# Kernel tuning notes

Hardware: AMD Instinct MI355X
Metric: run time of the kernel (lower is better)

The kernel has to match this reference:

```python
import jax, jax.numpy as jnp
import numpy as np

B, G, P, E, H, K = 16, 512, 512, 256, 16, 16
CLIP = 10.0

def setup_inputs() -> dict:
    key = jax.random.key(0)
    ks = jax.random.split(key, 10)
    d = {
        "input1": jax.random.normal(ks[0], (B, 1, E), jnp.float32),
        "input2": jax.random.normal(ks[1], (B, G, E), jnp.float32),
        "current_time": jax.random.uniform(ks[2], (B, G, 1), jnp.float32),
        "ninf_mask": jnp.zeros((B, G, P), jnp.float32),
        "encoded_nodes": jax.random.normal(ks[3], (B, P, E), jnp.float32),
        # learned params (Linear weights stored [in, out]; y = x @ W)
        "Wq": jax.random.normal(ks[4], (2 * E + 1, H * K), jnp.float32) / np.sqrt(2 * E + 1),
        "Wk": jax.random.normal(ks[5], (E, H * K), jnp.float32) / np.sqrt(E),
        "Wv": jax.random.normal(ks[6], (E, H * K), jnp.float32) / np.sqrt(E),
        "Wc_w": jax.random.normal(ks[7], (H * K, E), jnp.float32) / np.sqrt(H * K),
        "Wc_b": jax.random.normal(ks[8], (E,), jnp.float32) * 0.01,
    }
    return d

def _heads(x):  # [B, N, H*K] -> [B, H, N, K]
    b, n, _ = x.shape
    return x.reshape(b, n, H, K).transpose(0, 2, 1, 3)

def reference(input1, input2, current_time, ninf_mask, encoded_nodes, Wq, Wk, Wv, Wc_w, Wc_b):
    # reset(): precompute k, v, single_head_key from encoded_nodes
    k = _heads(encoded_nodes @ Wk)  # [B,H,P,K]
    v = _heads(encoded_nodes @ Wv)  # [B,H,P,K]

    # forward()
    input_cat = jnp.concatenate(
        (jnp.broadcast_to(input1, (B, G, E)), input2, current_time), axis=2)  # [B,G,2E+1]
    q = _heads(input_cat @ Wq)  # [B,H,G,K]

    # MHA with additive ninf mask
    score = jnp.einsum("bhgk,bhpk->bhgp", q, k) / np.sqrt(K)
    score = score + ninf_mask[:, None, :, :]
    weights = jax.nn.softmax(score, axis=3)
    out = jnp.einsum("bhgp,bhpk->bhgk", weights, v)
    out_concat = out.transpose(0, 2, 1, 3).reshape(B, G, H * K)
    mh_atten_out = out_concat @ Wc_w + Wc_b  # [B,G,E]

    # single-head pointer score with tanh clipping
    score2 = jnp.einsum("bge,bpe->bgp", mh_atten_out, encoded_nodes) / np.sqrt(E)
    score_clipped = CLIP * jnp.tanh(score2)
    probs = jax.nn.softmax(score_clipped + ninf_mask, axis=2)
    return probs
```

## Files before the change

### kernel.cpp

```cpp
#include <hip/hip_runtime.h>
#include <math.h>

#define BB 16
#define GG 512
#define PP 512
#define EE 256
#define HH 16
#define KD 16
#define HK 256

typedef __bf16 bf16x8 __attribute__((ext_vector_type(8)));
typedef __bf16 bf16x4 __attribute__((ext_vector_type(4)));
typedef float f32x4 __attribute__((ext_vector_type(4)));
typedef float f32x16 __attribute__((ext_vector_type(16)));
typedef int i32x4 __attribute__((ext_vector_type(4)));

#define SA_STRIDE 40
#define SMEM_BYTES 30720

__device__ inline void cvt_split8(const float* __restrict__ p, bf16x8& h, bf16x8& l)
{
    float4 f0 = *(const float4*)p;
    float4 f1 = *(const float4*)(p + 4);
    float v[8] = {f0.x, f0.y, f0.z, f0.w, f1.x, f1.y, f1.z, f1.w};
#pragma unroll
    for (int j = 0; j < 8; ++j) {
        __bf16 hh = (__bf16)v[j];
        h[j] = hh;
        l[j] = (__bf16)(v[j] - (float)hh);
    }
}

__device__ inline int cvt_pk_bf16(float lo, float hi)
{
    int r;
    asm("v_cvt_pk_bf16_f32 %0, %1, %2" : "=v"(r) : "v"(lo), "v"(hi));
    return r;
}

__device__ inline void w2proj_body(int bx, int tid, unsigned char* smem,
                                   const float* __restrict__ enc,
                                   const float* __restrict__ Wc,
                                   const float* __restrict__ bias,
                                   __bf16* __restrict__ W2th,
                                   __bf16* __restrict__ W2tl,
                                   float* __restrict__ biasEnc)
{
    __bf16* sAh = (__bf16*)smem;
    __bf16* sAl = sAh + 64 * SA_STRIDE;
    __bf16* sBh = sAl + 64 * SA_STRIDE;
    __bf16* sBl = sBh + 64 * SA_STRIDE;

    const int lane = tid & 63;
    const int w = __builtin_amdgcn_readfirstlane(tid >> 6);
    const int b  = bx >> 5;
    const int t  = bx & 31;
    const int p0 = (t >> 2) * 64;
    const int n0 = (t & 3) * 64;
    const bool do_bias = (n0 == 0);
    const int wm = (w >> 1) * 32, wn = (w & 1) * 32;
    const int ln = lane & 15, kq = (lane >> 4) * 8;
    const int ar = tid >> 2, ac = (tid & 3) * 8;

    f32x4 acc[2][2];
#pragma unroll
    for (int i = 0; i < 2; ++i)
#pragma unroll
        for (int j = 0; j < 2; ++j) acc[i][j] = (f32x4){0.f, 0.f, 0.f, 0.f};
    float bacc = 0.f;

    for (int k0 = 0; k0 < EE; k0 += 32) {
        {
            const float* ap = enc + ((size_t)(b * PP + p0 + ar)) * EE + k0 + ac;
            float4 f0 = *(const float4*)ap;
            float4 f1 = *(const float4*)(ap + 4);
            float v[8] = {f0.x, f0.y, f0.z, f0.w, f1.x, f1.y, f1.z, f1.w};
            bf16x8 h8, l8;
#pragma unroll
            for (int j = 0; j < 8; ++j) {
                __bf16 hh = (__bf16)v[j];
                h8[j] = hh;
                l8[j] = (__bf16)(v[j] - (float)hh);
            }
            if (do_bias) {
#pragma unroll
                for (int j = 0; j < 8; ++j) bacc += v[j] * bias[k0 + ac + j];
            }
            *(bf16x8*)&sAh[ar * SA_STRIDE + ac] = h8;
            *(bf16x8*)&sAl[ar * SA_STRIDE + ac] = l8;
        }
        {
            bf16x8 h8, l8;
            cvt_split8(Wc + (size_t)(n0 + ar) * EE + k0 + ac, h8, l8);
            *(bf16x8*)&sBh[ar * SA_STRIDE + ac] = h8;
            *(bf16x8*)&sBl[ar * SA_STRIDE + ac] = l8;
        }
        __syncthreads();

        bf16x8 ah[2], al[2];
#pragma unroll
        for (int mt = 0; mt < 2; ++mt) {
            ah[mt] = *(const bf16x8*)&sAh[(wm + mt * 16 + ln) * SA_STRIDE + kq];
            al[mt] = *(const bf16x8*)&sAl[(wm + mt * 16 + ln) * SA_STRIDE + kq];
        }
#pragma unroll
        for (int nt = 0; nt < 2; ++nt) {
            const int rowb = wn + nt * 16 + ln;
            bf16x8 bh8 = *(const bf16x8*)&sBh[rowb * SA_STRIDE + kq];
            bf16x8 bl8 = *(const bf16x8*)&sBl[rowb * SA_STRIDE + kq];
#pragma unroll
            for (int mt = 0; mt < 2; ++mt) {
                acc[mt][nt] = __builtin_amdgcn_mfma_f32_16x16x32_bf16(ah[mt], bh8, acc[mt][nt], 0, 0, 0);
                acc[mt][nt] = __builtin_amdgcn_mfma_f32_16x16x32_bf16(al[mt], bh8, acc[mt][nt], 0, 0, 0);
                acc[mt][nt] = __builtin_amdgcn_mfma_f32_16x16x32_bf16(ah[mt], bl8, acc[mt][nt], 0, 0, 0);
            }
        }
        __syncthreads();
    }

    if (do_bias) {
        bacc += __shfl_xor(bacc, 1);
        bacc += __shfl_xor(bacc, 2);
        if ((tid & 3) == 0) biasEnc[b * PP + p0 + ar] = bacc;
    }

    const int rbase = (lane >> 4) * 4;
#pragma unroll
    for (int mt = 0; mt < 2; ++mt)
#pragma unroll
        for (int nt = 0; nt < 2; ++nt)
#pragma unroll
            for (int r = 0; r < 4; ++r) {
                const int p = p0 + wm + mt * 16 + rbase + r;
                const int n = n0 + wn + nt * 16 + ln;
                const float v = acc[mt][nt][r];
                const __bf16 h = (__bf16)v;
                const size_t o = ((size_t)(b * PP + p)) * HK + n;
                W2th[o] = h;
                W2tl[o] = (__bf16)(v - (float)h);
            }
}

__global__ __launch_bounds__(256) void weight_prep(const float* __restrict__ Wk,
                                                   const float* __restrict__ Wv,
                                                   const float* __restrict__ Wq,
                                                   const float* __restrict__ Wc,
                                                   const float* __restrict__ in1,
                                                   const float* __restrict__ enc,
                                                   const float* __restrict__ Wcb,
                                                   __bf16* __restrict__ wkt_h, __bf16* __restrict__ wkt_l,
                                                   __bf16* __restrict__ wvt_h, __bf16* __restrict__ wvt_l,
                                                   __bf16* __restrict__ wqt_h, __bf16* __restrict__ wqt_l,
                                                   float* __restrict__ q1p,
                                                   __bf16* __restrict__ W2th, __bf16* __restrict__ W2tl,
                                                   float* __restrict__ biasEnc)
{
    __shared__ __align__(16) unsigned char smem[4 * 64 * SA_STRIDE * 2];
    if (blockIdx.x < 512) {
        w2proj_body(blockIdx.x, threadIdx.x, smem, enc, Wc, Wcb, W2th, W2tl, biasEnc);
        return;
    }
    int gid = (blockIdx.x - 512) * 256 + threadIdx.x;
    if (gid < 16384) {
        const int b = gid >> 10, q = (gid >> 8) & 3, n = gid & 255;
        const float* ip = in1 + (size_t)b * EE + q * 64;
        const float* wp = Wq + (size_t)(q * 64) * HK + n;
        float acc = 0.f;
#pragma unroll 8
        for (int k = 0; k < 64; ++k) acc += ip[k] * wp[(size_t)k * HK];
        q1p[gid] = acc;
        return;
    }
    int id = gid - 16384;
    if (id >= 196608) return;
    const float* W;
    __bf16 *th, *tl;
    int krow = 0;
    if (id < 65536)       { W = Wk; th = wkt_h; tl = wkt_l; }
    else if (id < 131072) { id -= 65536;  W = Wv; th = wvt_h; tl = wvt_l; }
    else                  { id -= 131072; W = Wq; th = wqt_h; tl = wqt_l; krow = 256; }
    const int k = id & 255;
    const int n = id >> 8;
    const float v = W[(size_t)(k + krow) * HK + n];
    const __bf16 h = (__bf16)v;
    th[(n << 8) + k] = h;
    tl[(n << 8) + k] = (__bf16)(v - (float)h);
}

__device__ inline void kvproj_body(int bx, int tid, unsigned char* smem,
                                   const float* __restrict__ A,
                                   const __bf16* __restrict__ Bkh,
                                   const __bf16* __restrict__ Bkl,
                                   const __bf16* __restrict__ Bvh,
                                   const __bf16* __restrict__ Bvl,
                                   __bf16* __restrict__ Khi,
                                   __bf16* __restrict__ Klo,
                                   __bf16* __restrict__ Vt)
{
    __bf16* sAh = (__bf16*)smem;
    __bf16* sAl = sAh + 64 * SA_STRIDE;
    __bf16* sB  = sAl + 64 * SA_STRIDE;

    const int lane = tid & 63;
    const int w = __builtin_amdgcn_readfirstlane(tid >> 6);
    const int m0 = (bx >> 2) * 64;
    const int n0 = (bx & 3) * 64;
    const int wm = (w >> 1) * 32, wn = (w & 1) * 32;
    const int ln = lane & 15, kq = (lane >> 4) * 8;
    const int ar = tid >> 2, ac = (tid & 3) * 8;

    const __bf16* bsel = (w == 0) ? Bkh : (w == 1) ? Bkl : (w == 2) ? Bvh : Bvl;

    f32x4 ak[2][2], av[2][2];
#pragma unroll
    for (int i = 0; i < 2; ++i)
#pragma unroll
        for (int j = 0; j < 2; ++j) {
            ak[i][j] = (f32x4){0.f, 0.f, 0.f, 0.f};
            av[i][j] = (f32x4){0.f, 0.f, 0.f, 0.f};
        }

    for (int k0 = 0; k0 < EE; k0 += 32) {
        {
            bf16x8 h8, l8;
            cvt_split8(A + (size_t)(m0 + ar) * EE + k0 + ac, h8, l8);
            *(bf16x8*)&sAh[ar * SA_STRIDE + ac] = h8;
            *(bf16x8*)&sAl[ar * SA_STRIDE + ac] = l8;
        }
        {
            const __bf16* src = bsel + (size_t)(n0 + lane) * EE + k0;
            __bf16* dst = sB + (w * 64 + lane) * SA_STRIDE;
            *(bf16x8*)&dst[0]  = *(const bf16x8*)&src[0];
            *(bf16x8*)&dst[8]  = *(const bf16x8*)&src[8];
            *(bf16x8*)&dst[16] = *(const bf16x8*)&src[16];
            *(bf16x8*)&dst[24] = *(const bf16x8*)&src[24];
        }
        __syncthreads();

        bf16x8 ah[2], al[2];
#pragma unroll
        for (int mt = 0; mt < 2; ++mt) {
            ah[mt] = *(const bf16x8*)&sAh[(wm + mt * 16 + ln) * SA_STRIDE + kq];
            al[mt] = *(const bf16x8*)&sAl[(wm + mt * 16 + ln) * SA_STRIDE + kq];
        }
#pragma unroll
        for (int nt = 0; nt < 2; ++nt) {
            const int rowb = wn + nt * 16 + ln;
            bf16x8 bkh8 = *(const bf16x8*)&sB[(0 * 64 + rowb) * SA_STRIDE + kq];
            bf16x8 bkl8 = *(const bf16x8*)&sB[(1 * 64 + rowb) * SA_STRIDE + kq];
            bf16x8 bvh8 = *(const bf16x8*)&sB[(2 * 64 + rowb) * SA_STRIDE + kq];
            bf16x8 bvl8 = *(const bf16x8*)&sB[(3 * 64 + rowb) * SA_STRIDE + kq];
#pragma unroll
            for (int mt = 0; mt < 2; ++mt) {
                ak[mt][nt] = __builtin_amdgcn_mfma_f32_16x16x32_bf16(ah[mt], bkh8, ak[mt][nt], 0, 0, 0);
                ak[mt][nt] = __builtin_amdgcn_mfma_f32_16x16x32_bf16(al[mt], bkh8, ak[mt][nt], 0, 0, 0);
                ak[mt][nt] = __builtin_amdgcn_mfma_f32_16x16x32_bf16(ah[mt], bkl8, ak[mt][nt], 0, 0, 0);
                av[mt][nt] = __builtin_amdgcn_mfma_f32_16x16x32_bf16(ah[mt], bvh8, av[mt][nt], 0, 0, 0);
                av[mt][nt] = __builtin_amdgcn_mfma_f32_16x16x32_bf16(al[mt], bvh8, av[mt][nt], 0, 0, 0);
                av[mt][nt] = __builtin_amdgcn_mfma_f32_16x16x32_bf16(ah[mt], bvl8, av[mt][nt], 0, 0, 0);
            }
        }
        __syncthreads();
    }

    __bf16* eKh = (__bf16*)smem;
    __bf16* eKl = eKh + 5120;
    __bf16* eV  = eKl + 5120;

    const int rbase = (lane >> 4) * 4;
#pragma unroll
    for (int mt = 0; mt < 2; ++mt)
#pragma unroll
        for (int nt = 0; nt < 2; ++nt) {
            const int hloc = (w & 1) * 2 + nt;
            const int nl = wn + nt * 16 + ln;
#pragma unroll
            for (int r = 0; r < 4; ++r) {
                const int m = wm + mt * 16 + rbase + r;
                const float vk = ak[mt][nt][r];
                const __bf16 hk = (__bf16)vk;
                eKh[(hloc * 64 + m) * 20 + ln] = hk;
                eKl[(hloc * 64 + m) * 20 + ln] = (__bf16)(vk - (float)hk);
                eV[nl * 68 + m] = (__bf16)av[mt][nt][r];
            }
        }
    __syncthreads();

    const int b = m0 >> 9;
    const int pbase = m0 & (PP - 1);
    {
        const int hl = tid >> 6, p = tid & 63;
        const int hg = (n0 >> 4) + hl;
        const size_t dst = (((size_t)b * HH + hg) * PP + pbase + p) * KD;
        const int base = (hl * 64 + p) * 20;
        uint2 a0 = *(const uint2*)&eKh[base + 0];
        uint2 a1 = *(const uint2*)&eKh[base + 4];
        uint2 a2 = *(const uint2*)&eKh[base + 8];
        uint2 a3 = *(const uint2*)&eKh[base + 12];
        *(uint4*)(Khi + dst)     = make_uint4(a0.x, a0.y, a1.x, a1.y);
        *(uint4*)(Khi + dst + 8) = make_uint4(a2.x, a2.y, a3.x, a3.y);
        uint2 c0 = *(const uint2*)&eKl[base + 0];
        uint2 c1 = *(const uint2*)&eKl[base + 4];
        uint2 c2 = *(const uint2*)&eKl[base + 8];
        uint2 c3 = *(const uint2*)&eKl[base + 12];
        *(uint4*)(Klo + dst)     = make_uint4(c0.x, c0.y, c1.x, c1.y);
        *(uint4*)(Klo + dst + 8) = make_uint4(c2.x, c2.y, c3.x, c3.y);
    }
    {
        const int n = tid >> 2, qq = tid & 3;
        const int ng = n0 + n, hg = ng >> 4, kk = ng & 15;
        const int base = n * 68 + qq * 16;
        uint2 v0 = *(const uint2*)&eV[base + 0];
        uint2 v1 = *(const uint2*)&eV[base + 4];
        uint2 v2 = *(const uint2*)&eV[base + 8];
        uint2 v3 = *(const uint2*)&eV[base + 12];
        const size_t dst = ((((size_t)b * HH + hg) * KD + kk) * PP) + pbase + qq * 16;
        *(uint4*)(Vt + dst)     = make_uint4(v0.x, v0.y, v1.x, v1.y);
        *(uint4*)(Vt + dst + 8) = make_uint4(v2.x, v2.y, v3.x, v3.y);
    }
}

__device__ inline void qproj_body(int bx, int tid, unsigned char* smem,
                                  const float* __restrict__ in2,
                                  const float* __restrict__ ct,
                                  const __bf16* __restrict__ Bh,
                                  const __bf16* __restrict__ Bl,
                                  const float* __restrict__ WqFull,
                                  const float* __restrict__ q1p,
                                  __bf16* __restrict__ Qhi,
                                  __bf16* __restrict__ Qlo)
{
    __bf16* sAh = (__bf16*)smem;
    __bf16* sAl = sAh + 64 * SA_STRIDE;
    __bf16* sB  = sAl + 64 * SA_STRIDE;

    const int lane = tid & 63;
    const int w = __builtin_amdgcn_readfirstlane(tid >> 6);
    const int m0 = (bx >> 2) * 64;
    const int n0 = (bx & 3) * 64;
    const int wm = (w >> 1) * 32, wn = (w & 1) * 32;
    const int ln = lane & 15, kq = (lane >> 4) * 8;
    const int ar = tid >> 2, ac = (tid & 3) * 8;
    const int b = m0 >> 9;
    const float* WqLast = WqFull + (size_t)512 * HK;

    f32x4 acc[2][2];
#pragma unroll
    for (int i = 0; i < 2; ++i)
#pragma unroll
        for (int j = 0; j < 2; ++j) acc[i][j] = (f32x4){0.f, 0.f, 0.f, 0.f};

    for (int k0 = 0; k0 < EE; k0 += 32) {
        {
            bf16x8 h8, l8;
            cvt_split8(in2 + (size_t)(m0 + ar) * EE + k0 + ac, h8, l8);
            *(bf16x8*)&sAh[ar * SA_STRIDE + ac] = h8;
            *(bf16x8*)&sAl[ar * SA_STRIDE + ac] = l8;
        }
        {
            const int mat = w >> 1;
            const int row = (w & 1) * 32 + (lane >> 1);
            const int half = (lane & 1) * 16;
            const __bf16* src = (mat ? Bl : Bh) + ((size_t)(n0 + row) << 8) + k0 + half;
            __bf16* dst = sB + (mat * 64 + row) * SA_STRIDE + half;
            *(bf16x8*)&dst[0] = *(const bf16x8*)&src[0];
            *(bf16x8*)&dst[8] = *(const bf16x8*)&src[8];
        }
        __syncthreads();

        bf16x8 ah[2], al[2];
#pragma unroll
        for (int mt = 0; mt < 2; ++mt) {
            ah[mt] = *(const bf16x8*)&sAh[(wm + mt * 16 + ln) * SA_STRIDE + kq];
            al[mt] = *(const bf16x8*)&sAl[(wm + mt * 16 + ln) * SA_STRIDE + kq];
        }
#pragma unroll
        for (int nt = 0; nt < 2; ++nt) {
            const int rowb = wn + nt * 16 + ln;
            bf16x8 bh8 = *(const bf16x8*)&sB[(0 * 64 + rowb) * SA_STRIDE + kq];
            bf16x8 bl8 = *(const bf16x8*)&sB[(1 * 64 + rowb) * SA_STRIDE + kq];
#pragma unroll
            for (int mt = 0; mt < 2; ++mt) {
                acc[mt][nt] = __builtin_amdgcn_mfma_f32_16x16x32_bf16(ah[mt], bh8, acc[mt][nt], 0, 0, 0);
                acc[mt][nt] = __builtin_amdgcn_mfma_f32_16x16x32_bf16(al[mt], bh8, acc[mt][nt], 0, 0, 0);
                acc[mt][nt] = __builtin_amdgcn_mfma_f32_16x16x32_bf16(ah[mt], bl8, acc[mt][nt], 0, 0, 0);
            }
        }
        __syncthreads();
    }

    __bf16* eQh = (__bf16*)smem;
    __bf16* eQl = eQh + 5120;

    const int rbase = (lane >> 4) * 4;
#pragma unroll
    for (int mt = 0; mt < 2; ++mt)
#pragma unroll
        for (int nt = 0; nt < 2; ++nt) {
            const int hloc = (w & 1) * 2 + nt;
            const int ng = n0 + wn + nt * 16 + ln;
            const float wq = WqLast[ng];
            const float q1v = q1p[b * 1024 + 0 * 256 + ng] + q1p[b * 1024 + 1 * 256 + ng]
                            + q1p[b * 1024 + 2 * 256 + ng] + q1p[b * 1024 + 3 * 256 + ng];
#pragma unroll
            for (int r = 0; r < 4; ++r) {
                const int m = wm + mt * 16 + rbase + r;
                const float v = acc[mt][nt][r] + q1v + ct[m0 + m] * wq;
                const __bf16 h = (__bf16)v;
                eQh[(hloc * 64 + m) * 20 + ln] = h;
                eQl[(hloc * 64 + m) * 20 + ln] = (__bf16)(v - (float)h);
            }
        }
    __syncthreads();

    {
        const int hl = tid >> 6, p = tid & 63;
        const int hg = (n0 >> 4) + hl;
        const int g = (m0 & (GG - 1)) + p;
        const size_t dst = (((size_t)b * HH + hg) * GG + g) * KD;
        const int base = (hl * 64 + p) * 20;
        uint2 a0 = *(const uint2*)&eQh[base + 0];
        uint2 a1 = *(const uint2*)&eQh[base + 4];
        uint2 a2 = *(const uint2*)&eQh[base + 8];
        uint2 a3 = *(const uint2*)&eQh[base + 12];
        *(uint4*)(Qhi + dst)     = make_uint4(a0.x, a0.y, a1.x, a1.y);
        *(uint4*)(Qhi + dst + 8) = make_uint4(a2.x, a2.y, a3.x, a3.y);
        uint2 c0 = *(const uint2*)&eQl[base + 0];
        uint2 c1 = *(const uint2*)&eQl[base + 4];
        uint2 c2 = *(const uint2*)&eQl[base + 8];
        uint2 c3 = *(const uint2*)&eQl[base + 12];
        *(uint4*)(Qlo + dst)     = make_uint4(c0.x, c0.y, c1.x, c1.y);
        *(uint4*)(Qlo + dst + 8) = make_uint4(c2.x, c2.y, c3.x, c3.y);
    }
}

__global__ __launch_bounds__(256, 2) void fused_proj(const float* __restrict__ enc,
                                                     const __bf16* __restrict__ Bkh,
                                                     const __bf16* __restrict__ Bkl,
                                                     const __bf16* __restrict__ Bvh,
                                                     const __bf16* __restrict__ Bvl,
                                                     __bf16* __restrict__ Khi,
                                                     __bf16* __restrict__ Klo,
                                                     __bf16* __restrict__ Vt,
                                                     const float* __restrict__ in2,
                                                     const float* __restrict__ ct,
                                                     const __bf16* __restrict__ Bqh,
                                                     const __bf16* __restrict__ Bql,
                                                     const float* __restrict__ WqFull,
                                                     const float* __restrict__ q1p,
                                                     __bf16* __restrict__ Qhi,
                                                     __bf16* __restrict__ Qlo)
{
    __shared__ __align__(16) unsigned char smem[SMEM_BYTES];
    const int id = blockIdx.x;
    if (id < 512)
        kvproj_body(id, threadIdx.x, smem, enc, Bkh, Bkl, Bvh, Bvl, Khi, Klo, Vt);
    else
        qproj_body(id - 512, threadIdx.x, smem, in2, ct, Bqh, Bql, WqFull, q1p, Qhi, Qlo);
}

#define AT_STRIDE 264
#define MSK_STRIDE 516

__global__ __launch_bounds__(1024, 4) void attn_ptr(const __bf16* __restrict__ Qhi,
                                                    const __bf16* __restrict__ Qlo,
                                                    const __bf16* __restrict__ Khi,
                                                    const __bf16* __restrict__ Klo,
                                                    const __bf16* __restrict__ Vt,
                                                    const __bf16* __restrict__ w2_hi,
                                                    const __bf16* __restrict__ w2_lo,
                                                    const float* __restrict__ biasEnc,
                                                    const float* __restrict__ mask,
                                                    float* __restrict__ out)
{
    __shared__ __align__(16) float smask[32][MSK_STRIDE];
    __shared__ float srs[16][32];
    __shared__ __align__(16) __bf16 sAth[32][AT_STRIDE];
    __shared__ __align__(16) __bf16 sAtl[32][AT_STRIDE];

    const int t = threadIdx.x;
    const int lane = t & 63;
    const int w = __builtin_amdgcn_readfirstlane(t >> 6);
    const int id = blockIdx.x;
    const int b = id & 15;
    const int g0 = (id >> 4) * 32;
    const int ln32 = lane & 31;
    const int half = lane >> 5;
    const int h = w;

    {
        const float* msrc = mask + ((size_t)(b * GG + g0)) * PP;
#pragma unroll
        for (int i = 0; i < 4; ++i) {
            const int c = (t + i * 1024) * 4;
            const int row = c >> 9, col = c & 511;
            *(float4*)&smask[row][col] = *(const float4*)&msrc[row * 512 + col];
        }
    }
    __syncthreads();

    const size_t qbase = (((size_t)b * HH + h) * GG + g0) * KD;
    const size_t kbase = ((size_t)b * HH + h) * PP * KD;
    const size_t vbase = ((size_t)b * HH + h) * KD * PP;

    bf16x8 qah = *(const bf16x8*)(Qhi + qbase + (size_t)ln32 * KD + half * 8);
    bf16x8 qal = *(const bf16x8*)(Qlo + qbase + (size_t)ln32 * KD + half * 8);

    float rs = 0.f;
    f32x16 acc = (f32x16){0.f, 0.f, 0.f, 0.f, 0.f, 0.f, 0.f, 0.f,
                          0.f, 0.f, 0.f, 0.f, 0.f, 0.f, 0.f, 0.f};
    const int dv = ln32 & 15;

#pragma unroll 4
    for (int pc = 0; pc < 16; ++pc) {
        const int pb = pc * 32;
        const size_t ko = kbase + (size_t)(pb + ln32) * KD + half * 8;
        bf16x8 kh = *(const bf16x8*)(Khi + ko);
        bf16x8 kl = *(const bf16x8*)(Klo + ko);
        bf16x8 vb0 = *(const bf16x8*)(Vt + vbase + (size_t)dv * PP + pb + half * 8);
        bf16x8 vb1 = *(const bf16x8*)(Vt + vbase + (size_t)dv * PP + pb + 16 + half * 8);

        f32x16 s = (f32x16){0.f, 0.f, 0.f, 0.f, 0.f, 0.f, 0.f, 0.f,
                            0.f, 0.f, 0.f, 0.f, 0.f, 0.f, 0.f, 0.f};
        __builtin_amdgcn_s_setprio(1);
        s = __builtin_amdgcn_mfma_f32_32x32x16_bf16(kh, qah, s, 0, 0, 0);
        s = __builtin_amdgcn_mfma_f32_32x32x16_bf16(kh, qal, s, 0, 0, 0);
        s = __builtin_amdgcn_mfma_f32_32x32x16_bf16(kl, qah, s, 0, 0, 0);
        __builtin_amdgcn_s_setprio(0);

        const float4 m0 = *(const float4*)&smask[ln32][pb + 0  + 4 * half];
        const float4 m1 = *(const float4*)&smask[ln32][pb + 8  + 4 * half];
        const float4 m2 = *(const float4*)&smask[ln32][pb + 16 + 4 * half];
        const float4 m3 = *(const float4*)&smask[ln32][pb + 24 + 4 * half];
        s[0]  = __expf(s[0]  * 0.25f + m0.x);
        s[1]  = __expf(s[1]  * 0.25f + m0.y);
        s[2]  = __expf(s[2]  * 0.25f + m0.z);
        s[3]  = __expf(s[3]  * 0.25f + m0.w);
        s[4]  = __expf(s[4]  * 0.25f + m1.x);
        s[5]  = __expf(s[5]  * 0.25f + m1.y);
        s[6]  = __expf(s[6]  * 0.25f + m1.z);
        s[7]  = __expf(s[7]  * 0.25f + m1.w);
        s[8]  = __expf(s[8]  * 0.25f + m2.x);
        s[9]  = __expf(s[9]  * 0.25f + m2.y);
        s[10] = __expf(s[10] * 0.25f + m2.z);
        s[11] = __expf(s[11] * 0.25f + m2.w);
        s[12] = __expf(s[12] * 0.25f + m3.x);
        s[13] = __expf(s[13] * 0.25f + m3.y);
        s[14] = __expf(s[14] * 0.25f + m3.z);
        s[15] = __expf(s[15] * 0.25f + m3.w);
#pragma unroll
        for (int r = 0; r < 16; ++r) rs += s[r];

        const int w01 = cvt_pk_bf16(s[0],  s[1]);
        const int w23 = cvt_pk_bf16(s[2],  s[3]);
        const int w45 = cvt_pk_bf16(s[4],  s[5]);
        const int w67 = cvt_pk_bf16(s[6],  s[7]);
        const int w89 = cvt_pk_bf16(s[8],  s[9]);
        const int wAB = cvt_pk_bf16(s[10], s[11]);
        const int wCD = cvt_pk_bf16(s[12], s[13]);
        const int wEF = cvt_pk_bf16(s[14], s[15]);
        const int x1 = half ? w01 : w45;
        const int x2 = half ? w23 : w67;
        const int x3 = half ? w89 : wCD;
        const int x4 = half ? wAB : wEF;
        const int p1 = __shfl_xor(x1, 32);
        const int p2 = __shfl_xor(x2, 32);
        const int p3 = __shfl_xor(x3, 32);
        const int p4 = __shfl_xor(x4, 32);
        i32x4 f0 = half ? (i32x4){p1, p2, w45, w67} : (i32x4){w01, w23, p1, p2};
        i32x4 f1 = half ? (i32x4){p3, p4, wCD, wEF} : (i32x4){w89, wAB, p3, p4};
        bf16x8 pa0 = *(bf16x8*)&f0;
        bf16x8 pa1 = *(bf16x8*)&f1;

        __builtin_amdgcn_s_setprio(1);
        acc = __builtin_amdgcn_mfma_f32_32x32x16_bf16(pa0, vb0, acc, 0, 0, 0);
        acc = __builtin_amdgcn_mfma_f32_32x32x16_bf16(pa1, vb1, acc, 0, 0, 0);
        __builtin_amdgcn_s_setprio(0);
    }

    rs += __shfl_xor(rs, 32);
    if (half == 0) srs[w][ln32] = rs;

    if (ln32 < 16) {
#pragma unroll
        for (int r = 0; r < 16; ++r) {
            const int g = (r & 3) + 8 * (r >> 2) + 4 * half;
            const float v = acc[r] / srs[w][g];
            const __bf16 hv = (__bf16)v;
            sAth[g][w * 16 + ln32] = hv;
            sAtl[g][w * 16 + ln32] = (__bf16)(v - (float)hv);
        }
    }
    __syncthreads();

    const size_t brow = ((size_t)(b * PP + w * 32 + ln32)) * HK + half * 8;
    const float be = biasEnc[b * PP + w * 32 + ln32];

    f32x16 acc0 = (f32x16){0.f, 0.f, 0.f, 0.f, 0.f, 0.f, 0.f, 0.f,
                           0.f, 0.f, 0.f, 0.f, 0.f, 0.f, 0.f, 0.f};
    f32x16 acc1 = acc0, acc2 = acc0;

#pragma unroll 4
    for (int kc = 0; kc < HK; kc += 16) {
        bf16x8 ah = *(const bf16x8*)&sAth[ln32][kc + half * 8];
        bf16x8 al = *(const bf16x8*)&sAtl[ln32][kc + half * 8];
        bf16x8 bh = *(const bf16x8*)(w2_hi + brow + kc);
        bf16x8 bl = *(const bf16x8*)(w2_lo + brow + kc);
        __builtin_amdgcn_s_setprio(1);
        acc0 = __builtin_amdgcn_mfma_f32_32x32x16_bf16(ah, bh, acc0, 0, 0, 0);
        acc1 = __builtin_amdgcn_mfma_f32_32x32x16_bf16(al, bh, acc1, 0, 0, 0);
        acc2 = __builtin_amdgcn_mfma_f32_32x32x16_bf16(ah, bl, acc2, 0, 0, 0);
        __builtin_amdgcn_s_setprio(0);
    }

    f32x16 pacc = acc0 + acc1 + acc2;

    float rsum[16];
#pragma unroll
    for (int r = 0; r < 16; ++r) {
        const int row = (r & 3) + 8 * (r >> 2) + 4 * half;
        float sc = (pacc[r] + be) * 0.0625f;
        sc = fminf(9.f, fmaxf(-9.f, sc));
        const float e2 = __expf(2.f * sc);
        const float th = (e2 - 1.f) / (e2 + 1.f);
        const float m = smask[row][w * 32 + ln32];
        const float e = __expf(10.f * th + m);
        pacc[r] = e;
        rsum[r] = e;
    }

#pragma unroll
    for (int r = 0; r < 16; ++r) {
        rsum[r] += __shfl_xor(rsum[r], 1);
        rsum[r] += __shfl_xor(rsum[r], 2);
        rsum[r] += __shfl_xor(rsum[r], 4);
        rsum[r] += __shfl_xor(rsum[r], 8);
        rsum[r] += __shfl_xor(rsum[r], 16);
    }
    if (ln32 == 0) {
#pragma unroll
        for (int r = 0; r < 16; ++r)
            srs[w][(r & 3) + 8 * (r >> 2) + 4 * half] = rsum[r];
    }
    __syncthreads();

    float inv[16];
#pragma unroll
    for (int r = 0; r < 16; ++r) {
        const int row = (r & 3) + 8 * (r >> 2) + 4 * half;
        float tot = 0.f;
#pragma unroll
        for (int wv = 0; wv < 16; ++wv) tot += srs[wv][row];
        inv[r] = 1.f / tot;
    }

#pragma unroll
    for (int r = 0; r < 16; ++r) {
        const int row = (r & 3) + 8 * (r >> 2) + 4 * half;
        out[((size_t)(b * GG + g0 + row)) * PP + w * 32 + ln32] = pacc[r] * inv[r];
    }
}

extern "C" void kernel_launch(void* const* d_in, const int* in_sizes, int n_in,
                              void* d_out, int out_size, void* d_ws, size_t ws_size,
                              hipStream_t stream)
{
    const float* in1  = (const float*)d_in[0];
    const float* in2  = (const float*)d_in[1];
    const float* ct   = (const float*)d_in[2];
    const float* mask = (const float*)d_in[3];
    const float* enc  = (const float*)d_in[4];
    const float* Wq   = (const float*)d_in[5];
    const float* Wk   = (const float*)d_in[6];
    const float* Wv   = (const float*)d_in[7];
    const float* Wcw  = (const float*)d_in[8];
    const float* Wcb  = (const float*)d_in[9];
    float* out = (float*)d_out;
    float* ws  = (float*)d_ws;

    const size_t SEG = (size_t)BB * GG * HK;
    __bf16* Khi = (__bf16*)ws;
    __bf16* Klo = Khi + SEG;
    __bf16* Vt  = (__bf16*)(ws + SEG);
    __bf16* Qhi = (__bf16*)(ws + 2 * SEG);
    __bf16* Qlo = Qhi + SEG;
    __bf16* wkt_h = (__bf16*)(ws + 3 * SEG);
    __bf16* wkt_l = wkt_h + 65536;
    __bf16* wvt_h = wkt_l + 65536;
    __bf16* wvt_l = wvt_h + 65536;
    __bf16* wqt_h = wvt_l + 65536;
    __bf16* wqt_l = wqt_h + 65536;
    float*  q1p     = ws + 3 * SEG + 196608;
    float*  biasEnc = q1p + 16384;
    __bf16* W2th  = (__bf16*)(ws + 4 * SEG);
    __bf16* W2tl  = W2th + SEG;

    const dim3 blk(256);

    weight_prep<<<dim3(1344), blk, 0, stream>>>(Wk, Wv, Wq, Wcw, in1, enc, Wcb,
                                                wkt_h, wkt_l, wvt_h, wvt_l,
                                                wqt_h, wqt_l, q1p,
                                                W2th, W2tl, biasEnc);

    fused_proj<<<dim3(1024), blk, 0, stream>>>(enc, wkt_h, wkt_l, wvt_h, wvt_l,
                                               Khi, Klo, Vt,
                                               in2, ct, wqt_h, wqt_l, Wq, q1p,
                                               Qhi, Qlo);

    attn_ptr<<<dim3(256), dim3(1024), 0, stream>>>(Qhi, Qlo, Khi, Klo, Vt,
                                                   W2th, W2tl, biasEnc, mask, out);
}
```

Baseline: 175.2 us.

## Split fused K/V projection blocks into separate K and V blocks

The combined K/V projection body is split into separate K and V bodies, each computing a single hi/lo-split GEMM. The B-tile load is remapped so that four waves cover two matrices instead of four. This shrinks shared memory per block from 30 KB to 20 KB, raises the launch-bounds occupancy hint from 2 to 3, and grows the grid from 1024 to 1536 blocks to expose more parallelism. In exchange, the encoder tile is loaded and split into bf16 hi/lo parts twice, once for K and once for V, which adds redundant global reads and conversion work.

```diff
diff --git a/kernel.cpp b/kernel.cpp
--- a/kernel.cpp
+++ b/kernel.cpp
@@ -16,7 +16,7 @@
 typedef int i32x4 __attribute__((ext_vector_type(4)));
 
 #define SA_STRIDE 40
-#define SMEM_BYTES 30720
+#define SMEM_BYTES 20480
 
 __device__ inline void cvt_split8(const float* __restrict__ p, bf16x8& h, bf16x8& l)
 {
@@ -187,15 +187,12 @@
     tl[(n << 8) + k] = (__bf16)(v - (float)h);
 }
 
-__device__ inline void kvproj_body(int bx, int tid, unsigned char* smem,
-                                   const float* __restrict__ A,
-                                   const __bf16* __restrict__ Bkh,
-                                   const __bf16* __restrict__ Bkl,
-                                   const __bf16* __restrict__ Bvh,
-                                   const __bf16* __restrict__ Bvl,
-                                   __bf16* __restrict__ Khi,
-                                   __bf16* __restrict__ Klo,
-                                   __bf16* __restrict__ Vt)
+__device__ inline void kproj_body(int bx, int tid, unsigned char* smem,
+                                  const float* __restrict__ A,
+                                  const __bf16* __restrict__ Bh,
+                                  const __bf16* __restrict__ Bl,
+                                  __bf16* __restrict__ Khi,
+                                  __bf16* __restrict__ Klo)
 {
     __bf16* sAh = (__bf16*)smem;
     __bf16* sAl = sAh + 64 * SA_STRIDE;
@@ -209,16 +206,11 @@
     const int ln = lane & 15, kq = (lane >> 4) * 8;
     const int ar = tid >> 2, ac = (tid & 3) * 8;
 
-    const __bf16* bsel = (w == 0) ? Bkh : (w == 1) ? Bkl : (w == 2) ? Bvh : Bvl;
-
-    f32x4 ak[2][2], av[2][2];
+    f32x4 acc[2][2];
 #pragma unroll
     for (int i = 0; i < 2; ++i)
 #pragma unroll
-        for (int j = 0; j < 2; ++j) {
-            ak[i][j] = (f32x4){0.f, 0.f, 0.f, 0.f};
-            av[i][j] = (f32x4){0.f, 0.f, 0.f, 0.f};
-        }
+        for (int j = 0; j < 2; ++j) acc[i][j] = (f32x4){0.f, 0.f, 0.f, 0.f};
 
     for (int k0 = 0; k0 < EE; k0 += 32) {
         {
@@ -228,12 +220,13 @@
             *(bf16x8*)&sAl[ar * SA_STRIDE + ac] = l8;
         }
         {
-            const __bf16* src = bsel + (size_t)(n0 + lane) * EE + k0;
-            __bf16* dst = sB + (w * 64 + lane) * SA_STRIDE;
-            *(bf16x8*)&dst[0]  = *(const bf16x8*)&src[0];
-            *(bf16x8*)&dst[8]  = *(const bf16x8*)&src[8];
-            *(bf16x8*)&dst[16] = *(const bf16x8*)&src[16];
-            *(bf16x8*)&dst[24] = *(const bf16x8*)&src[24];
+            const int mat = w >> 1;
+            const int row = (w & 1) * 32 + (lane >> 1);
+            const int halfk = (lane & 1) * 16;
+            const __bf16* src = (mat ? Bl : Bh) + ((size_t)(n0 + row) << 8) + k0 + halfk;
+            __bf16* dst = sB + (mat * 64 + row) * SA_STRIDE + halfk;
+            *(bf16x8*)&dst[0] = *(const bf16x8*)&src[0];
+            *(bf16x8*)&dst[8] = *(const bf16x8*)&src[8];
         }
         __syncthreads();
 
@@ -246,18 +239,13 @@
 #pragma unroll
         for (int nt = 0; nt < 2; ++nt) {
             const int rowb = wn + nt * 16 + ln;
-            bf16x8 bkh8 = *(const bf16x8*)&sB[(0 * 64 + rowb) * SA_STRIDE + kq];
-            bf16x8 bkl8 = *(const bf16x8*)&sB[(1 * 64 + rowb) * SA_STRIDE + kq];
-            bf16x8 bvh8 = *(const bf16x8*)&sB[(2 * 64 + rowb) * SA_STRIDE + kq];
-            bf16x8 bvl8 = *(const bf16x8*)&sB[(3 * 64 + rowb) * SA_STRIDE + kq];
+            bf16x8 bh8 = *(const bf16x8*)&sB[(0 * 64 + rowb) * SA_STRIDE + kq];
+            bf16x8 bl8 = *(const bf16x8*)&sB[(1 * 64 + rowb) * SA_STRIDE + kq];
 #pragma unroll
             for (int mt = 0; mt < 2; ++mt) {
-                ak[mt][nt] = __builtin_amdgcn_mfma_f32_16x16x32_bf16(ah[mt], bkh8, ak[mt][nt], 0, 0, 0);
-                ak[mt][nt] = __builtin_amdgcn_mfma_f32_16x16x32_bf16(al[mt], bkh8, ak[mt][nt], 0, 0, 0);
-                ak[mt][nt] = __builtin_amdgcn_mfma_f32_16x16x32_bf16(ah[mt], bkl8, ak[mt][nt], 0, 0, 0);
-                av[mt][nt] = __builtin_amdgcn_mfma_f32_16x16x32_bf16(ah[mt], bvh8, av[mt][nt], 0, 0, 0);
-                av[mt][nt] = __builtin_amdgcn_mfma_f32_16x16x32_bf16(al[mt], bvh8, av[mt][nt], 0, 0, 0);
-                av[mt][nt] = __builtin_amdgcn_mfma_f32_16x16x32_bf16(ah[mt], bvl8, av[mt][nt], 0, 0, 0);
+                acc[mt][nt] = __builtin_amdgcn_mfma_f32_16x16x32_bf16(ah[mt], bh8, acc[mt][nt], 0, 0, 0);
+                acc[mt][nt] = __builtin_amdgcn_mfma_f32_16x16x32_bf16(al[mt], bh8, acc[mt][nt], 0, 0, 0);
+                acc[mt][nt] = __builtin_amdgcn_mfma_f32_16x16x32_bf16(ah[mt], bl8, acc[mt][nt], 0, 0, 0);
             }
         }
         __syncthreads();
@@ -265,7 +253,6 @@
 
     __bf16* eKh = (__bf16*)smem;
     __bf16* eKl = eKh + 5120;
-    __bf16* eV  = eKl + 5120;
 
     const int rbase = (lane >> 4) * 4;
 #pragma unroll
@@ -273,15 +260,13 @@
 #pragma unroll
         for (int nt = 0; nt < 2; ++nt) {
             const int hloc = (w & 1) * 2 + nt;
-            const int nl = wn + nt * 16 + ln;
 #pragma unroll
             for (int r = 0; r < 4; ++r) {
                 const int m = wm + mt * 16 + rbase + r;
-                const float vk = ak[mt][nt][r];
+                const float vk = acc[mt][nt][r];
                 const __bf16 hk = (__bf16)vk;
                 eKh[(hloc * 64 + m) * 20 + ln] = hk;
                 eKl[(hloc * 64 + m) * 20 + ln] = (__bf16)(vk - (float)hk);
-                eV[nl * 68 + m] = (__bf16)av[mt][nt][r];
             }
         }
     __syncthreads();
@@ -306,6 +291,89 @@
         *(uint4*)(Klo + dst)     = make_uint4(c0.x, c0.y, c1.x, c1.y);
         *(uint4*)(Klo + dst + 8) = make_uint4(c2.x, c2.y, c3.x, c3.y);
     }
+}
+
+__device__ inline void vproj_body(int bx, int tid, unsigned char* smem,
+                                  const float* __restrict__ A,
+                                  const __bf16* __restrict__ Bh,
+                                  const __bf16* __restrict__ Bl,
+                                  __bf16* __restrict__ Vt)
+{
+    __bf16* sAh = (__bf16*)smem;
+    __bf16* sAl = sAh + 64 * SA_STRIDE;
+    __bf16* sB  = sAl + 64 * SA_STRIDE;
+
+    const int lane = tid & 63;
+    const int w = __builtin_amdgcn_readfirstlane(tid >> 6);
+    const int m0 = (bx >> 2) * 64;
+    const int n0 = (bx & 3) * 64;
+    const int wm = (w >> 1) * 32, wn = (w & 1) * 32;
+    const int ln = lane & 15, kq = (lane >> 4) * 8;
+    const int ar = tid >> 2, ac = (tid & 3) * 8;
+
+    f32x4 acc[2][2];
+#pragma unroll
+    for (int i = 0; i < 2; ++i)
+#pragma unroll
+        for (int j = 0; j < 2; ++j) acc[i][j] = (f32x4){0.f, 0.f, 0.f, 0.f};
+
+    for (int k0 = 0; k0 < EE; k0 += 32) {
+        {
+            bf16x8 h8, l8;
+            cvt_split8(A + (size_t)(m0 + ar) * EE + k0 + ac, h8, l8);
+            *(bf16x8*)&sAh[ar * SA_STRIDE + ac] = h8;
+            *(bf16x8*)&sAl[ar * SA_STRIDE + ac] = l8;
+        }
+        {
+            const int mat = w >> 1;
+            const int row = (w & 1) * 32 + (lane >> 1);
+            const int halfk = (lane & 1) * 16;
+            const __bf16* src = (mat ? Bl : Bh) + ((size_t)(n0 + row) << 8) + k0 + halfk;
+            __bf16* dst = sB + (mat * 64 + row) * SA_STRIDE + halfk;
+            *(bf16x8*)&dst[0] = *(const bf16x8*)&src[0];
+            *(bf16x8*)&dst[8] = *(const bf16x8*)&src[8];
+        }
+        __syncthreads();
+
+        bf16x8 ah[2], al[2];
+#pragma unroll
+        for (int mt = 0; mt < 2; ++mt) {
+            ah[mt] = *(const bf16x8*)&sAh[(wm + mt * 16 + ln) * SA_STRIDE + kq];
+            al[mt] = *(const bf16x8*)&sAl[(wm + mt * 16 + ln) * SA_STRIDE + kq];
+        }
+#pragma unroll
+        for (int nt = 0; nt < 2; ++nt) {
+            const int rowb = wn + nt * 16 + ln;
+            bf16x8 bh8 = *(const bf16x8*)&sB[(0 * 64 + rowb) * SA_STRIDE + kq];
+            bf16x8 bl8 = *(const bf16x8*)&sB[(1 * 64 + rowb) * SA_STRIDE + kq];
+#pragma unroll
+            for (int mt = 0; mt < 2; ++mt) {
+                acc[mt][nt] = __builtin_amdgcn_mfma_f32_16x16x32_bf16(ah[mt], bh8, acc[mt][nt], 0, 0, 0);
+                acc[mt][nt] = __builtin_amdgcn_mfma_f32_16x16x32_bf16(al[mt], bh8, acc[mt][nt], 0, 0, 0);
+                acc[mt][nt] = __builtin_amdgcn_mfma_f32_16x16x32_bf16(ah[mt], bl8, acc[mt][nt], 0, 0, 0);
+            }
+        }
+        __syncthreads();
+    }
+
+    __bf16* eV = (__bf16*)smem;
+
+    const int rbase = (lane >> 4) * 4;
+#pragma unroll
+    for (int mt = 0; mt < 2; ++mt)
+#pragma unroll
+        for (int nt = 0; nt < 2; ++nt) {
+            const int nl = wn + nt * 16 + ln;
+#pragma unroll
+            for (int r = 0; r < 4; ++r) {
+                const int m = wm + mt * 16 + rbase + r;
+                eV[nl * 68 + m] = (__bf16)acc[mt][nt][r];
+            }
+        }
+    __syncthreads();
+
+    const int b = m0 >> 9;
+    const int pbase = m0 & (PP - 1);
     {
         const int n = tid >> 2, qq = tid & 3;
         const int ng = n0 + n, hg = ng >> 4, kk = ng & 15;
@@ -434,7 +502,7 @@
     }
 }
 
-__global__ __launch_bounds__(256, 2) void fused_proj(const float* __restrict__ enc,
+__global__ __launch_bounds__(256, 3) void fused_proj(const float* __restrict__ enc,
                                                      const __bf16* __restrict__ Bkh,
                                                      const __bf16* __restrict__ Bkl,
                                                      const __bf16* __restrict__ Bvh,
@@ -454,9 +522,11 @@
     __shared__ __align__(16) unsigned char smem[SMEM_BYTES];
     const int id = blockIdx.x;
     if (id < 512)
-        kvproj_body(id, threadIdx.x, smem, enc, Bkh, Bkl, Bvh, Bvl, Khi, Klo, Vt);
+        kproj_body(id, threadIdx.x, smem, enc, Bkh, Bkl, Khi, Klo);
+    else if (id < 1024)
+        vproj_body(id - 512, threadIdx.x, smem, enc, Bvh, Bvl, Vt);
     else
-        qproj_body(id - 512, threadIdx.x, smem, in2, ct, Bqh, Bql, WqFull, q1p, Qhi, Qlo);
+        qproj_body(id - 1024, threadIdx.x, smem, in2, ct, Bqh, Bql, WqFull, q1p, Qhi, Qlo);
 }
 
 #define AT_STRIDE 264
@@ -702,7 +772,7 @@
                                                 wqt_h, wqt_l, q1p,
                                                 W2th, W2tl, biasEnc);
 
-    fused_proj<<<dim3(1024), blk, 0, stream>>>(enc, wkt_h, wkt_l, wvt_h, wvt_l,
+    fused_proj<<<dim3(1536), blk, 0, stream>>>(enc, wkt_h, wkt_l, wvt_h, wvt_l,
                                                Khi, Klo, Vt,
                                                in2, ct, wqt_h, wqt_l, Wq, q1p,
                                                Qhi, Qlo);
```

Result: no change. 172.5 us (-1.5%).
